# Optimization experiments

Measured on AMD Instinct MI355X. Metric: run time of the kernel, lower is better.

Reference implementation:

```python
import jax, jax.numpy as jnp
import numpy as np
from jax import lax

E = 10        # embed_dim
SEQ = 4000    # input_frame (sample_length=40)
G = 800       # group
F = 5         # frames_in_group
B = 16
VOCAB = 8192


def _conv2d(x, w, b):
    # x: [B, C, H, W], w: [O, I, 3, 3], padding=1 -> SAME
    y = lax.conv_general_dilated(x, w, (1, 1), 'SAME',
                                 dimension_numbers=('NCHW', 'OIHW', 'NCHW'))
    return y + b[None, :, None, None]


def _conv1d_k1(x, w, b):
    # Conv1d(seq, seq, kernel=1): x [B, S, L], w [S_out, S_in]
    return jnp.einsum('oi,bil->bol', w, x) + b[None, :, None]


def _linear(x, w, b):
    # torch Linear: w [out, in]
    return x @ w.T + b


def setup_inputs() -> dict:
    key = jax.random.key(0)
    ks = jax.random.split(key, 24)
    s = 0.02
    inp = {
        'X': jax.random.randint(ks[0], (B, SEQ, 15), 0, VOCAB),
        'emb_table': jax.random.normal(ks[1], (VOCAB, E), jnp.float32),
        'w_dwc_lsp': jax.random.normal(ks[2], (G, G, 3, 3), jnp.float32) * s,
        'b_dwc_lsp': jnp.zeros((G,), jnp.float32),
        'w_dwc_other': jax.random.normal(ks[3], (G, G, 3, 3), jnp.float32) * s,
        'b_dwc_other': jnp.zeros((G,), jnp.float32),
        'w_local': jax.random.normal(ks[4], (SEQ, SEQ), jnp.float32) * s,
        'b_local': jnp.zeros((SEQ,), jnp.float32),
        'w_global': jax.random.normal(ks[5], (SEQ, SEQ), jnp.float32) * s,
        'b_global': jnp.zeros((SEQ,), jnp.float32),
        'w_gq': jax.random.normal(ks[6], (4 * E, 4 * E), jnp.float32) * s,
        'b_gq': jnp.zeros((4 * E,), jnp.float32),
        'w_cq': jax.random.normal(ks[7], (4 * E, 4 * E), jnp.float32) * s,
        'b_cq': jnp.zeros((4 * E,), jnp.float32),
        'w_pq': jax.random.normal(ks[8], (4 * E, 3 * E), jnp.float32) * s,
        'b_pq': jnp.zeros((4 * E,), jnp.float32),
        'w_lk': jax.random.normal(ks[9], (4 * E, 4 * E), jnp.float32) * s,
        'b_lk': jnp.zeros((4 * E,), jnp.float32),
        'w_lv': jax.random.normal(ks[10], (4 * E, 4 * E), jnp.float32) * s,
        'b_lv': jnp.zeros((4 * E,), jnp.float32),
        'w_cls': jax.random.normal(ks[11], (1, SEQ * 4 * E * 3), jnp.float32) * 0.001,
        'b_cls': jnp.zeros((1,), jnp.float32),
        'bn_w': jnp.ones((1,), jnp.float32),
        'bn_b': jnp.zeros((1,), jnp.float32),
    }
    return inp


def reference(X, emb_table, w_dwc_lsp, b_dwc_lsp, w_dwc_other, b_dwc_other,
              w_local, b_local, w_global, b_global,
              w_gq, b_gq, w_cq, b_cq, w_pq, b_pq,
              w_lk, b_lk, w_lv, b_lv, w_cls, b_cls, bn_w, bn_b):
    batch, seq, cw = X.shape
    gamma = jnp.float32(0.8)
    pk = jnp.array([0, 0, 0, 0, 1, 3, 1, 2, 3, 2, 3, 1, 2, 3, 3], jnp.float32)
    D = jnp.repeat(gamma ** pk, E)  # [150]

    Xe = emb_table[X].reshape(batch, seq, cw * E) * D  # [B, S, 150]
    ch = Xe.reshape(batch, seq, cw, E)                  # 15 chunks of E

    lsp = ch[:, :, jnp.array([0, 1, 2, 3])].reshape(batch, seq, 4 * E)
    pitch = ch[:, :, jnp.array([4, 5, 10])].reshape(batch, seq, 3 * E)
    code = ch[:, :, jnp.array([6, 7, 11, 12])].reshape(batch, seq, 4 * E)
    gain = ch[:, :, jnp.array([8, 13, 9, 14])].reshape(batch, seq, 4 * E)

    conv_lsp = _conv2d(lsp.reshape(batch, G, F, 4 * E), w_dwc_lsp, b_dwc_lsp).reshape(batch, seq, 4 * E)
    conv_pitch = _conv2d(pitch.reshape(batch, G, F, 3 * E), w_dwc_other, b_dwc_other).reshape(batch, seq, 3 * E)
    conv_code = _conv2d(code.reshape(batch, G, F, 4 * E), w_dwc_other, b_dwc_other).reshape(batch, seq, 4 * E)
    conv_gain = _conv2d(gain.reshape(batch, G, F, 4 * E), w_dwc_other, b_dwc_other).reshape(batch, seq, 4 * E)

    conv_lsp = _conv1d_k1(conv_lsp, w_local, b_local)
    conv_pitch = _conv1d_k1(conv_pitch, w_local, b_local)
    conv_code = _conv1d_k1(conv_code, w_local, b_local)
    conv_gain = _conv1d_k1(conv_gain, w_local, b_local)

    gain_q = _linear(conv_gain, w_gq, b_gq)    # [B, S, 40]
    pitch_q = _linear(conv_pitch, w_pq, b_pq)  # [B, S, 40]
    code_q = _linear(conv_code, w_cq, b_cq)    # [B, S, 40]
    lsp_k = _linear(conv_lsp, w_lk, b_lk)
    lsp_v = _linear(conv_lsp, w_lv, b_lv)

    # Q @ K^T @ V with no softmax: associate as Q @ (K^T V), O(S*d^2)
    kv = jnp.einsum('bsd,bse->bde', lsp_k, lsp_v)  # [B, 40, 40]
    out_gain = jnp.einsum('bsd,bde->bse', gain_q, kv) + lsp
    out_pitch = jnp.einsum('bsd,bde->bse', pitch_q, kv) + lsp
    out_code = jnp.einsum('bsd,bde->bse', code_q, kv) + lsp

    atten_out = jnp.concatenate([out_gain, out_pitch, out_code], -1)  # [B, S, 120]
    gf = _conv1d_k1(atten_out, w_global, b_global).reshape(batch, -1)  # [B, 480000]

    y = gf @ w_cls.T + b_cls  # [B, 1]
    # BatchNorm1d(1) in eval mode: running_mean=0, running_var=1
    eps = jnp.float32(1e-5)
    y = y * (bn_w / jnp.sqrt(1.0 + eps)) + bn_b
    return jax.nn.sigmoid(y)
```

## Files before the change

### kernel.cpp

```cpp
#include <hip/hip_runtime.h>
#include <hip/hip_bf16.h>

typedef _Float16 f16;
typedef __attribute__((ext_vector_type(8))) _Float16 half8;
typedef __attribute__((ext_vector_type(4))) _Float16 half4;
typedef __attribute__((ext_vector_type(4))) float f32x4;

static const int BN = 16, SEQN = 4000;

__device__ __forceinline__ void gload_lds(f16* lds, const f16* g) {
  __builtin_amdgcn_global_load_lds((const __attribute__((address_space(1))) unsigned int*)g,
                                   (__attribute__((address_space(3))) unsigned int*)lds, 16, 0, 0);
}

__device__ __forceinline__ int xcd_swz(int orig, int nwg) {
  int q = nwg >> 3, r = nwg & 7, x = orig & 7, o = orig >> 3;
  return (x < r ? x * (q + 1) : r * (q + 1) + (x - r) * q) + o;
}

__device__ __forceinline__ void body_wconv(char* SM, int o,
    const float* __restrict__ w_dwc_l, f16* __restrict__ wp_lsp) {
  float* sh = (float*)SM;
  int t = threadIdx.x;
  for (int p4 = t; p4 < 1800; p4 += 256)
    *(f32x4*)&sh[p4 * 4] = *(const f32x4*)&w_dwc_l[(long)o * 7200 + p4 * 4];
  __syncthreads();
  for (int c = t; c < 912; c += 256) {
    int p = c * 8;
    int seg = p / 2432, r = p - seg * 2432;
    half8 h = {};
    if (r < 2400) {
      int de = r / 800, gib = r - de * 800;
#pragma unroll
      for (int j = 0; j < 8; j++) h[j] = (f16)sh[(gib + j) * 9 + seg * 3 + de];
    }
    *(half8*)&wp_lsp[(long)o * 7296 + p] = h;
  }
}

__device__ __forceinline__ void body_wlocal(char* SM, int s,
    const float* __restrict__ w_local, f16* __restrict__ wlp) {
  float* sh = (float*)SM;
  int t = threadIdx.x;
  for (int p = t; p < 4000; p += 256) {
    int g = p / 5, f = p - g * 5;
    sh[f * 808 + g] = w_local[(long)s * 4000 + p];
  }
  __syncthreads();
  for (int c = t; c < 512; c += 256) {
    int p = c * 8;
    half8 h = {};
    if (p < 4000) {
      int f = p / 800, g = p - f * 800;
      const float* src = &sh[f * 808 + g];
#pragma unroll
      for (int j = 0; j < 8; j++) h[j] = (f16)src[j];
    }
    *(half8*)&wlp[(long)s * 4096 + p] = h;
  }
}

__device__ __forceinline__ void body_wcT(char* SM, int id,
    const float* __restrict__ w_cls, f16* __restrict__ wcT) {
  float (*tile)[33] = (float(*)[33])SM;
  int t = threadIdx.x;
  int c0 = (id % 4) * 32, r0 = (id / 4) * 32;
  int tx = t & 31, ty = t >> 5;
  for (int i = ty; i < 32; i += 8) {
    int r = r0 + i, c = c0 + tx;
    tile[i][tx] = (r < 4000 && c < 120) ? w_cls[(long)r * 120 + c] : 0.f;
  }
  __syncthreads();
  for (int i = ty; i < 32; i += 8) {
    int c = c0 + i, r = r0 + tx;
    if (c < 128 && r < 4000) wcT[(long)c * 4000 + r] = (f16)(tile[tx][i] * 1024.f);
  }
}

__device__ __forceinline__ void body_woT(char* SM, int id,
    const float* __restrict__ in, f16* __restrict__ out) {
  float (*sh)[292] = (float(*)[292])SM;
  int bg = id % 25, bgi = id / 25;
  int g0 = bg * 32, gi0 = bgi * 32;
  int t = threadIdx.x;
  for (int p = t; p < 2304; p += 256) {
    int gl = p / 72, q4 = p % 72;
    *(f32x4*)&sh[gl][q4 * 4] = *(const f32x4*)&in[(long)(g0 + gl) * 7200 + gi0 * 9 + q4 * 4];
  }
  __syncthreads();
  for (int c = t; c < 1152; c += 256) {
    int gl8 = c & 3, q = c >> 2;
    int gil = q & 31, z = q >> 5;
    half8 h;
#pragma unroll
    for (int j = 0; j < 8; j++) h[j] = (f16)sh[gl8 * 8 + j][gil * 9 + z];
    *(half8*)&out[(long)z * 640000 + (gi0 + gil) * 800 + g0 + gl8 * 8] = h;
  }
}

__device__ __forceinline__ void body_gather(char* SM, int bid,
    const int* __restrict__ X, const float* __restrict__ emb,
    f16* __restrict__ P_lsp, f16* __restrict__ P_pit,
    f16* __restrict__ P_cod, f16* __restrict__ P_gai,
    float* __restrict__ lsp32) {
  int* sx_ = (int*)SM;
  float* slsp = (float*)(SM + 9600);
  const float scale[15] = {1.f,1.f,1.f,1.f,0.8f,0.512f,0.8f,0.64f,0.512f,0.64f,0.512f,0.8f,0.64f,0.512f,0.512f};
  const int br[15] = {0,0,0,0,1,1,2,2,3,3,1,2,2,3,3};
  const int po[15] = {0,1,2,3,0,1,0,1,0,2,2,2,3,1,3};
  int t = threadIdx.x;
  int b = bid / 25, gc = bid % 25;
  int g0 = gc * 32, s0 = g0 * 5;
  const int* xbase = X + ((long)b * SEQN + s0) * 15;
  for (int p = t; p < 600; p += 256)
    *(f32x4*)&sx_[p * 4] = *(const f32x4*)&xbase[p * 4];
  __syncthreads();
  for (int it = t; it < 2400; it += 256) {
    int gl = it & 31, q = it >> 5, f = q % 5, c = q / 5;
    int idx = sx_[(gl * 5 + f) * 15 + c];
    const float* er = emb + (long)idx * 10;
    int ty = br[c], p = po[c];
    f16* P = (ty == 0) ? P_lsp : (ty == 1) ? P_pit : (ty == 2) ? P_cod : P_gai;
    int Wp = (ty == 1) ? 32 : 42;
    f16* base = P + ((long)((f + 1) * 16 + b) * Wp + (1 + p * 10)) * 800 + g0 + gl;
    float sc = scale[c];
#pragma unroll
    for (int j = 0; j < 10; j++) {
      float v = er[j] * sc;
      base[(long)j * 800] = (f16)v;
      if (ty == 0) slsp[(gl * 5 + f) * 40 + p * 10 + j] = v;
    }
  }
  __syncthreads();
  float* ldst = lsp32 + ((long)b * SEQN + s0) * 40;
  for (int p4 = t; p4 < 1600; p4 += 256)
    *(f32x4*)&ldst[p4 * 4] = *(const f32x4*)&slsp[p4 * 4];
}

__device__ __forceinline__ void body_c1(char* SM, int blk,
    const float* __restrict__ wcls, const float* __restrict__ bg,
    float* __restrict__ c1p) {
  float* red = (float*)SM;
  int t = threadIdx.x;
  float s = 0.f;
  for (long i = (long)blk * 256 + t; i < 480000; i += (long)120 * 256)
    s += wcls[i] * bg[i / 120];
  red[t] = s; __syncthreads();
  for (int o = 128; o > 0; o >>= 1) { if (t < o) red[t] += red[t + o]; __syncthreads(); }
  if (t == 0) c1p[blk] = red[0];
}

__device__ __forceinline__ void body_conv(char* SM, int id,
    const f16* __restrict__ P, const f16* __restrict__ wp, f16* __restrict__ Cp) {
  f16* Asb = (f16*)SM;
  f16* Bsb = Asb + 8192;
  int lin = xcd_swz(id % 175, 175);
  int z = id / 175;
  int df = z >> 1, hf = z & 1;
  int nx = lin % 7, my = lin / 7;
  int m0 = my * 128, n0 = nx * 128;
  Cp += (long)z * 2560000;
  int t = threadIdx.x;
  int gslot = (t & 3) ^ ((t >> 3) & 3);
  const f16 *ap[2], *bp[2];
#pragma unroll
  for (int q = 0; q < 2; q++) {
    int row = q * 64 + (t >> 2);
    int m = m0 + row;
    int f = m / 640, rem = m % 640, b = rem / 40, e = rem % 40;
    ap[q] = P + ((long)((f + df) * 16 + b) * 42 + e) * 800 + hf * 1216 + gslot * 8;
    bp[q] = wp + (long)(n0 + row) * 7296 + df * 2432 + hf * 1216 + gslot * 8;
  }
  int lane = t & 63, wv = t >> 6, l15 = lane & 15, kg = lane >> 4;
  int wm = (wv >> 1) * 64, wn = (wv & 1) * 64;
  int so = (kg ^ ((l15 >> 1) & 3)) << 3;
  f32x4 acc[4][4] = {};
  gload_lds(&Asb[t * 8], ap[0]); gload_lds(&Asb[2048 + t * 8], ap[1]);
  gload_lds(&Bsb[t * 8], bp[0]); gload_lds(&Bsb[2048 + t * 8], bp[1]);
  __syncthreads();
  int cur = 0;
  for (int kt = 0; kt < 38; kt++) {
    if (kt + 1 < 38) {
      int o = (kt + 1) * 32, nb = cur ^ 1;
      gload_lds(&Asb[nb * 4096 + t * 8], ap[0] + o); gload_lds(&Asb[nb * 4096 + 2048 + t * 8], ap[1] + o);
      gload_lds(&Bsb[nb * 4096 + t * 8], bp[0] + o); gload_lds(&Bsb[nb * 4096 + 2048 + t * 8], bp[1] + o);
    }
    half8 av[4], bv[4];
#pragma unroll
    for (int i = 0; i < 4; i++) av[i] = *(const half8*)&Asb[cur * 4096 + (wm + i * 16 + l15) * 32 + so];
#pragma unroll
    for (int j = 0; j < 4; j++) bv[j] = *(const half8*)&Bsb[cur * 4096 + (wn + j * 16 + l15) * 32 + so];
#pragma unroll
    for (int i = 0; i < 4; i++)
#pragma unroll
      for (int j = 0; j < 4; j++)
        acc[i][j] = __builtin_amdgcn_mfma_f32_16x16x32_f16(av[i], bv[j], acc[i][j], 0, 0, 0);
    __syncthreads();
    cur ^= 1;
  }
#pragma unroll
  for (int i = 0; i < 4; i++) {
    int mb = m0 + wm + i * 16 + kg * 4;
#pragma unroll
    for (int j = 0; j < 4; j++) {
      int n = n0 + wn + j * 16 + l15;
      if (n >= 800) continue;
      f32x4 d = acc[i][j];
#pragma unroll
      for (int r = 0; r < 4; r++)
        Cp[(long)(mb + r) * 800 + n] = (f16)d[r];
    }
  }
}

template <int OUTF16>
__device__ __forceinline__ void body_gemm128(char* SM, int x, int ky, int z,
    const f16* __restrict__ A, int lda, const f16* __restrict__ Bm, int ldb,
    float* __restrict__ C, f16* __restrict__ C16, int ldc,
    int gx, int nwg, int nkt, int KTtot, long cslice, long az, long bz, long cz,
    int Mreal, int Nreal, int Aclamp) {
  f16* Asb = (f16*)SM;
  f16* Bsb = Asb + 8192;
  A += (long)z * az;
  Bm += (long)z * bz;
  if (OUTF16) C16 += (long)z * cz + (long)ky * cslice;
  else C += (long)z * cz + (long)ky * cslice;
  int lin = xcd_swz(x, nwg);
  int nx = lin % gx, my = lin / gx;
  int m0 = my * 128, n0 = nx * 128;
  int kt0 = ky * nkt;
  int ktn = nkt; if (kt0 + ktn > KTtot) ktn = KTtot - kt0;
  int t = threadIdx.x;
  int gslot = (t & 3) ^ ((t >> 3) & 3);
  const f16 *ap[2], *bp[2];
#pragma unroll
  for (int q = 0; q < 2; q++) {
    int row = q * 64 + (t >> 2);
    int ra = m0 + row; if (ra >= Aclamp) ra = Aclamp - 1;
    ap[q] = A + (long)ra * lda + (long)kt0 * 32 + gslot * 8;
    bp[q] = Bm + (long)(n0 + row) * ldb + (long)kt0 * 32 + gslot * 8;
  }
  int lane = t & 63, wv = t >> 6, l15 = lane & 15, kg = lane >> 4;
  int wm = (wv >> 1) * 64, wn = (wv & 1) * 64;
  int so = (kg ^ ((l15 >> 1) & 3)) << 3;
  f32x4 acc[4][4] = {};
  gload_lds(&Asb[t * 8], ap[0]); gload_lds(&Asb[2048 + t * 8], ap[1]);
  gload_lds(&Bsb[t * 8], bp[0]); gload_lds(&Bsb[2048 + t * 8], bp[1]);
  __syncthreads();
  int cur = 0;
  for (int kt = 0; kt < ktn; kt++) {
    if (kt + 1 < ktn) {
      int o = (kt + 1) * 32, nb = cur ^ 1;
      gload_lds(&Asb[nb * 4096 + t * 8], ap[0] + o); gload_lds(&Asb[nb * 4096 + 2048 + t * 8], ap[1] + o);
      gload_lds(&Bsb[nb * 4096 + t * 8], bp[0] + o); gload_lds(&Bsb[nb * 4096 + 2048 + t * 8], bp[1] + o);
    }
    half8 av[4], bv[4];
#pragma unroll
    for (int i = 0; i < 4; i++) av[i] = *(const half8*)&Asb[cur * 4096 + (wm + i * 16 + l15) * 32 + so];
#pragma unroll
    for (int j = 0; j < 4; j++) bv[j] = *(const half8*)&Bsb[cur * 4096 + (wn + j * 16 + l15) * 32 + so];
#pragma unroll
    for (int i = 0; i < 4; i++)
#pragma unroll
      for (int j = 0; j < 4; j++)
        acc[i][j] = __builtin_amdgcn_mfma_f32_16x16x32_f16(av[i], bv[j], acc[i][j], 0, 0, 0);
    __syncthreads();
    cur ^= 1;
  }
#pragma unroll
  for (int i = 0; i < 4; i++) {
    int mb = m0 + wm + i * 16 + kg * 4;
#pragma unroll
    for (int j = 0; j < 4; j++) {
      int n = n0 + wn + j * 16 + l15;
      if (n >= Nreal) continue;
      f32x4 d = acc[i][j];
#pragma unroll
      for (int r = 0; r < 4; r++) {
        int m = mb + r;
        if (m >= Mreal) continue;
        if (OUTF16) C16[(long)m * ldc + n] = (f16)d[r];
        else C[(long)m * ldc + n] = d[r];
      }
    }
  }
}

__device__ __forceinline__ void body_tn(char* SM, int id,
    const f16* __restrict__ A, int lda, const float* __restrict__ B, int ldb,
    float* __restrict__ C, int ldc, int nkt, int KTtot, long cslice,
    int Mreal, int Nreal) {
  f16* As = (f16*)SM;
  f16* Bs = As + 4096;
  int n0 = (id & 31) * 128;
  int ky = id >> 5;
  int kt0 = ky * nkt;
  int ktn = nkt; if (kt0 + ktn > KTtot) ktn = KTtot - kt0;
  C += (long)ky * cslice;
  int t = threadIdx.x;
  int gslot = (t & 3) ^ ((t >> 3) & 3);
  const f16 *ap0, *ap1;
  {
    int r0 = t >> 2, r1 = 64 + (t >> 2);
    if (r0 >= Mreal) r0 = Mreal - 1;
    if (r1 >= Mreal) r1 = Mreal - 1;
    ap0 = A + (long)r0 * lda + (long)kt0 * 32 + gslot * 8;
    ap1 = A + (long)r1 * lda + (long)kt0 * 32 + gslot * 8;
  }
  int lane = t & 63, wv = t >> 6;
  int wm = (wv >> 1) * 64, wn = (wv & 1) * 64;
  int l15 = lane & 15, kg = lane >> 4;
  int so = (kg ^ ((l15 >> 1) & 3)) << 3;
  f32x4 acc[4][4] = {};
  for (int kt = 0; kt < ktn; kt++) {
    float rb[4][4];
    int nli[4], kqi[4];
#pragma unroll
    for (int i = 0; i < 4; i++) {
      int idd = i * 256 + t;
      nli[i] = idd & 127; kqi[i] = idd >> 7;
      int gn = n0 + nli[i]; if (gn >= Nreal) gn = Nreal - 1;
      long kb = ((long)(kt0 + kt) * 32 + kqi[i] * 4);
#pragma unroll
      for (int j = 0; j < 4; j++) rb[i][j] = B[(kb + j) * ldb + gn];
    }
    __syncthreads();
    gload_lds(&As[t * 8], ap0 + kt * 32);
    gload_lds(&As[2048 + t * 8], ap1 + kt * 32);
#pragma unroll
    for (int i = 0; i < 4; i++) {
      half4 h = {(f16)rb[i][0], (f16)rb[i][1], (f16)rb[i][2], (f16)rb[i][3]};
      *(half4*)&Bs[nli[i] * 36 + kqi[i] * 4] = h;
    }
    __syncthreads();
    half8 av[4], bv[4];
#pragma unroll
    for (int i = 0; i < 4; i++) {
      av[i] = *(const half8*)(&As[(wm + i * 16 + l15) * 32 + so]);
      bv[i] = *(const half8*)(&Bs[(wn + i * 16 + l15) * 36 + kg * 8]);
    }
#pragma unroll
    for (int i = 0; i < 4; i++)
#pragma unroll
      for (int j = 0; j < 4; j++)
        acc[i][j] = __builtin_amdgcn_mfma_f32_16x16x32_f16(av[i], bv[j], acc[i][j], 0, 0, 0);
  }
#pragma unroll
  for (int i = 0; i < 4; i++) {
    int mb = wm + i * 16 + kg * 4;
#pragma unroll
    for (int j = 0; j < 4; j++) {
      int n = n0 + wn + j * 16 + l15;
      if (n >= Nreal) continue;
      f32x4 d = acc[i][j];
#pragma unroll
      for (int r = 0; r < 4; r++) {
        int m = mb + r;
        if (m >= Mreal) continue;
        C[(long)m * ldc + n] = d[r];
      }
    }
  }
}

__device__ __forceinline__ void body_co_red(long gid,
    const f16* __restrict__ Cp, const float* __restrict__ bias, f16* __restrict__ co) {
  if (gid >= 640000) return;
  int m = gid / 200, n4 = (gid % 200) * 4;
  long o = (long)m * 800 + n4;
  f32x4 s = *(const f32x4*)&bias[n4];
#pragma unroll
  for (int z = 0; z < 6; z++) {
    half4 h = *(const half4*)&Cp[(long)z * 2560000 + o];
    s += (f32x4){(float)h[0], (float)h[1], (float)h[2], (float)h[3]};
  }
  int f = m / 640, r2 = m % 640;
  half4 hh = {(f16)s[0], (f16)s[1], (f16)s[2], (f16)s[3]};
  *(half4*)&co[(long)r2 * 4000 + f * 800 + n4] = hh;
}

__device__ __forceinline__ void body_vred(int idb, int MODE,
    const float* __restrict__ vp, float* __restrict__ vout, f16* __restrict__ tout) {
  int x = idb & 15, ec = idb >> 4;
  int s = x * 256 + threadIdx.x;
  if (s >= 4000) return;
  int g = s / 5, f = s % 5;
  float sums[40];
#pragma unroll
  for (int eo = 0; eo < 40; eo++) {
    int e = ec * 40 + eo;
    float sum = 0.f;
#pragma unroll
    for (int z = 0; z < 10; z++) sum += vp[(long)z * 480000 + (long)e * 4000 + s];
    sums[eo] = sum;
    if (MODE == 0) tout[(long)e * 4000 + s] = (f16)sum;
    else tout[(long)(f * 120 + e) * 832 + g] = (f16)sum;
  }
#pragma unroll
  for (int q = 0; q < 10; q++)
    *(f32x4*)&vout[(long)s * 120 + ec * 40 + q * 4] = *(f32x4*)&sums[q * 4];
}

__device__ __forceinline__ void body_cl_red(long gid,
    const f16* __restrict__ Clp, const float* __restrict__ bl, float* __restrict__ cl) {
  if (gid >= 640000) return;
  int m = gid / 160, n4 = (gid % 160) * 4;
  long o = (long)m * 640 + n4;
  float b = bl[m];
  f32x4 s = {b, b, b, b};
#pragma unroll
  for (int z = 0; z < 4; z++) {
    half4 h = *(const half4*)&Clp[(long)z * 2560000 + o];
    s += (f32x4){(float)h[0], (float)h[1], (float)h[2], (float)h[3]};
  }
  *(f32x4*)&cl[o] = s;
}

__device__ __forceinline__ void body_resid(char* SM, int chunk, int b,
    const float* __restrict__ lsp32, const float* __restrict__ vmat,
    float* __restrict__ rpart) {
  float* red = (float*)SM;
  int t = threadIdx.x;
  int s0 = chunk * 160;
  float y = 0.f;
  for (int idx = t; idx < 1600; idx += 256) {
    int sr = idx / 10, d4 = idx % 10;
    const float* lp = lsp32 + ((long)b * SEQN + s0 + sr) * 40 + d4 * 4;
    const float* vp = vmat + (long)(s0 + sr) * 120 + d4 * 4;
    f32x4 l = *(const f32x4*)lp;
    f32x4 vs = *(const f32x4*)vp + *(const f32x4*)(vp + 40) + *(const f32x4*)(vp + 80);
    y += l[0] * vs[0] + l[1] * vs[1] + l[2] * vs[2] + l[3] * vs[3];
  }
  red[t] = y; __syncthreads();
  for (int o = 128; o > 0; o >>= 1) { if (t < o) red[t] += red[t + o]; __syncthreads(); }
  if (t == 0) rpart[b * 25 + chunk] = red[0];
}

__device__ __forceinline__ void body_kv(char* SM, int chunk, int b,
    const float* __restrict__ cl, const float* __restrict__ wlk, const float* __restrict__ blk,
    const float* __restrict__ wlv, const float* __restrict__ blv, float* __restrict__ kvp) {
  float* s_wk = (float*)SM;
  float* s_wv = s_wk + 1600;
  float* s_cl = s_wv + 1600;
  float* s_k  = s_cl + 320;
  float* s_v  = s_k + 320;
  int t = threadIdx.x;
  for (int p = t; p < 1600; p += 256) { s_wk[p] = wlk[p]; s_wv[p] = wlv[p]; }
  float acc[7] = {0.f, 0.f, 0.f, 0.f, 0.f, 0.f, 0.f};
  for (int c8 = 0; c8 < 20; c8++) {
    int sb = chunk * 160 + c8 * 8;
    __syncthreads();
    for (int p = t; p < 320; p += 256) {
      int sl = p / 40, e = p % 40;
      s_cl[sl * 40 + e] = cl[(long)(sb + sl) * 640 + b * 40 + e];
    }
    __syncthreads();
    for (int p = t; p < 640; p += 256) {
      int half = p / 320, q = p % 320, sl = q / 40, d = q % 40;
      const float* w = half ? s_wv : s_wk;
      float r = half ? blv[d] : blk[d];
      for (int e = 0; e < 40; e++) r += w[d * 40 + e] * s_cl[sl * 40 + e];
      if (half) s_v[sl * 40 + d] = r; else s_k[sl * 40 + d] = r;
    }
    __syncthreads();
    int ai = 0;
    for (int p = t; p < 1600; p += 256, ai++) {
      int d = p / 40, e = p % 40;
      float a = acc[ai];
      for (int sl = 0; sl < 8; sl++) a += s_k[sl * 40 + d] * s_v[sl * 40 + e];
      acc[ai] = a;
    }
  }
  int ai = 0;
  for (int p = t; p < 1600; p += 256, ai++)
    kvp[((long)(b * 25 + chunk)) * 1600 + p] = acc[ai];
}

__device__ __forceinline__ void body_consts(char* SM, int e,
    const float* __restrict__ Vt, const float* __restrict__ vmat,
    const float* __restrict__ bconv, const float* __restrict__ blocal,
    float* __restrict__ cbblv, float* __restrict__ svv) {
  float* r1 = (float*)SM;
  float* r2 = r1 + 256;
  int t = threadIdx.x;
  float a = 0.f, b = 0.f;
  for (int s = t; s < 4000; s += 256) {
    a += bconv[s / 5] * Vt[(long)s * 120 + e] + blocal[s] * vmat[(long)s * 120 + e];
    b += vmat[(long)s * 120 + e];
  }
  r1[t] = a; r2[t] = b; __syncthreads();
  for (int o = 128; o > 0; o >>= 1) {
    if (t < o) { r1[t] += r1[t + o]; r2[t] += r2[t + o]; }
    __syncthreads();
  }
  if (t == 0) { cbblv[e] = r1[0]; svv[e] = r2[0]; }
}

__device__ __forceinline__ void body_fold(long c8,
    const float* __restrict__ A9, f16* __restrict__ Bp) {
  long p = c8 * 8;
  if (p >= 7 * 120 * 2496) return;
  int fp = p / 299520;
  int r = p % 299520;
  int eg = r / 2496, k2 = r % 2496;
  int zk = k2 / 832, kk = k2 % 832;
  half8 h = {};
  if (kk < 800) {
#pragma unroll
    for (int j = 0; j < 8; j++) {
      float s = 0.f;
#pragma unroll
      for (int dh = 0; dh < 3; dh++) {
        int f = fp - dh;
        if (f >= 0 && f < 5)
          s += A9[((long)(dh * 3 + zk) * 640 + f * 120 + eg) * 800 + kk + j];
      }
      h[j] = (f16)s;
    }
  }
  *(half8*)&Bp[p] = h;
}

__device__ __forceinline__ void body_kvred(long gid,
    const float* __restrict__ kvp, float* __restrict__ kv) {
  if (gid >= 16 * 1600) return;
  int b = gid / 1600, p = gid % 1600;
  float s = 0.f;
  for (int c = 0; c < 25; c++) s += kvp[((long)(b * 25 + c)) * 1600 + p];
  kv[gid] = s;
}

__device__ __forceinline__ void body_U(char* SM, int id,
    const f16* __restrict__ Pg, const f16* __restrict__ Pp, const f16* __restrict__ Pc,
    const f16* __restrict__ Bp, float* __restrict__ Upart) {
  f16* Asb = (f16*)SM;
  f16* Bsb = Asb + 8192;
  int m0 = (id % 28) * 64;
  int y = id / 28, fp = y / 3, zk = y % 3;
  const f16* P; int seg0, jw, Wp, e0;
  if (m0 < 640)       { seg0 = 0;    jw = 40; Wp = 42; e0 = 0;  P = Pg; }
  else if (m0 < 1152) { seg0 = 640;  jw = 30; Wp = 32; e0 = 40; P = Pp; }
  else                { seg0 = 1152; jw = 40; Wp = 42; e0 = 80; P = Pc; }
  P += (long)fp * 16 * Wp * 800;
  int t = threadIdx.x;
  int gslot = (t & 7) ^ ((t >> 3) & 7);
  const f16 *ap[2], *bp[2];
#pragma unroll
  for (int q = 0; q < 2; q++) {
    int row = q * 32 + (t >> 3);
    int l = m0 + row - seg0; if (l >= 16 * jw) l = 0;
    ap[q] = P + ((long)(l / jw) * Wp + (l % jw)) * 800 + (long)zk * 800 + gslot * 8;
    int brow = row; if (e0 + brow > 119) brow = 119 - e0;
    bp[q] = Bp + ((long)fp * 120 + e0 + brow) * 2496 + zk * 832 + gslot * 8;
  }
  int lane = t & 63, wv = t >> 6, l15 = lane & 15, kg = lane >> 4;
  int sx = l15 & 7;
  f32x4 acc[3] = {};
  gload_lds(&Asb[t * 8], ap[0]); gload_lds(&Asb[2048 + t * 8], ap[1]);
  gload_lds(&Bsb[t * 8], bp[0]); gload_lds(&Bsb[2048 + t * 8], bp[1]);
  __syncthreads();
  int cur = 0;
  for (int kt = 0; kt < 13; kt++) {
    if (kt + 1 < 13) {
      int o = (kt + 1) * 64, nb = cur ^ 1;
      gload_lds(&Asb[nb * 4096 + t * 8], ap[0] + o); gload_lds(&Asb[nb * 4096 + 2048 + t * 8], ap[1] + o);
      gload_lds(&Bsb[nb * 4096 + t * 8], bp[0] + o); gload_lds(&Bsb[nb * 4096 + 2048 + t * 8], bp[1] + o);
    }
#pragma unroll
    for (int ks = 0; ks < 2; ks++) {
      int so = ((ks * 4 + kg) ^ sx) << 3;
      half8 av = *(const half8*)&Asb[cur * 4096 + (wv * 16 + l15) * 64 + so];
#pragma unroll
      for (int j = 0; j < 3; j++) {
        half8 bv = *(const half8*)&Bsb[cur * 4096 + (j * 16 + l15) * 64 + so];
        acc[j] = __builtin_amdgcn_mfma_f32_16x16x32_f16(av, bv, acc[j], 0, 0, 0);
      }
    }
    __syncthreads();
    cur ^= 1;
  }
#pragma unroll
  for (int j = 0; j < 3; j++) {
    int n = j * 16 + l15;
    if (n >= 40) continue;
    f32x4 d = acc[j];
#pragma unroll
    for (int r = 0; r < 4; r++) {
      int m = m0 + wv * 16 + kg * 4 + r;
      if (m - seg0 >= 16 * jw) continue;
      Upart[((long)y * 1792 + m) * 40 + n] = d[r];
    }
  }
}

__device__ __forceinline__ void body_ured(long gid,
    const float* __restrict__ Upart, const float* __restrict__ cbblv,
    float* __restrict__ Ufin) {
  if (gid >= 1792 * 40) return;
  int m = gid / 40, e = gid % 40;
  int e0 = m < 640 ? 0 : (m < 1152 ? 40 : 80);
  float s = cbblv[e0 + e];
  for (int y = 0; y < 21; y++) s += Upart[(long)y * 71680 + gid];
  Ufin[gid] = s;
}

__global__ __launch_bounds__(256) void k_phase0(
    const float* w_dwc_l, f16* wp_lsp, const float* w_cls, f16* wcT,
    const int* X, const float* emb, f16* P_lsp, f16* P_pit, f16* P_cod, f16* P_gai,
    float* lsp32, const float* b_global, float* c1p) {
  __shared__ __align__(16) char SM[35200];
  int bid = blockIdx.x;
  if (bid < 800) body_wconv(SM, bid, w_dwc_l, wp_lsp);
  else if (bid < 1300) body_wcT(SM, bid - 800, w_cls, wcT);
  else if (bid < 1700) body_gather(SM, bid - 1300, X, emb, P_lsp, P_pit, P_cod, P_gai, lsp32);
  else body_c1(SM, bid - 1700, w_cls, b_global, c1p);
}

__global__ __launch_bounds__(256) void k_phase1(
    const f16* P_lsp, const f16* wp_lsp, f16* Cp,
    const f16* wcT, const float* w_global, float* vpart,
    const float* w_local, f16* wlp) {
  __shared__ __align__(16) char SM[32768];
  int bid = blockIdx.x;
  if (bid < 1050) body_conv(SM, bid, P_lsp, wp_lsp, Cp);
  else if (bid < 1370) body_tn(SM, bid - 1050, wcT, 4000, w_global, 4000, vpart, 4000, 13, 125, 480000L, 120, 4000);
  else body_wlocal(SM, bid - 1370, w_local, wlp);
}

__global__ __launch_bounds__(256) void k_phase2(
    const f16* Cp, const float* b_dwc_l, f16* co,
    const float* vpart, float* vmat, f16* vT,
    const float* w_dwc_o, f16* woT) {
  __shared__ __align__(16) char SM[37376];
  int bid = blockIdx.x;
  if (bid < 2500) body_co_red((long)bid * 256 + threadIdx.x, Cp, b_dwc_l, co);
  else if (bid < 2548) body_vred(bid - 2500, 0, vpart, vmat, vT);
  else body_woT(SM, bid - 2548, w_dwc_o, woT);
}

__global__ __launch_bounds__(256) void k_phase3(
    const f16* wlp, const f16* co, f16* Clp,
    const f16* vT, const float* w_local, float* vpart,
    const float* lsp32, const float* vmat, float* rpart) {
  __shared__ __align__(16) char SM[32768];
  int bid = blockIdx.x;
  if (bid < 640) body_gemm128<1>(SM, bid % 160, bid / 160, 0, wlp, 4096, co, 4000, nullptr, Clp, 640,
                                 5, 160, 32, 128, 2560000L, 0, 0, 0, 4000, 640, 4000);
  else if (bid < 960) body_tn(SM, bid - 640, vT, 4000, w_local, 4000, vpart, 4000, 13, 125, 480000L, 120, 4000);
  else { int id = bid - 960; body_resid(SM, id % 25, id / 25, lsp32, vmat, rpart); }
}

__global__ __launch_bounds__(256) void k_phase4(
    const f16* Clp, const float* b_local, float* cl,
    const float* vpart, float* Vt, f16* vtT) {
  int bid = blockIdx.x;
  if (bid < 2500) body_cl_red((long)bid * 256 + threadIdx.x, Clp, b_local, cl);
  else body_vred(bid - 2500, 1, vpart, Vt, vtT);
}

__global__ __launch_bounds__(256) void k_phase5(
    const float* cl, const float* w_lk, const float* b_lk,
    const float* w_lv, const float* b_lv, float* kvp,
    const f16* vtT, const f16* woT, float* A9,
    const float* Vt, const float* vmat, const float* b_dwc_o, const float* b_local,
    float* cbblv, float* svv) {
  __shared__ __align__(16) char SM[32768];
  int bid = blockIdx.x;
  if (bid < 400) body_kv(SM, bid % 25, bid / 25, cl, w_lk, b_lk, w_lv, b_lv, kvp);
  else if (bid < 715) { int id = bid - 400; body_gemm128<0>(SM, id % 35, 0, id / 35, vtT, 832, woT, 800, A9, nullptr, 800,
                                                             7, 35, 26, 26, 0L, 0, 640000, 512000, 600, 800, 600); }
  else body_consts(SM, bid - 715, Vt, vmat, b_dwc_o, b_local, cbblv, svv);
}

__global__ __launch_bounds__(256) void k_phase6(
    const float* A9, f16* Bp, const float* kvp, float* kvb) {
  int bid = blockIdx.x;
  if (bid < 1024) body_fold((long)bid * 256 + threadIdx.x, A9, Bp);
  else body_kvred((long)(bid - 1024) * 256 + threadIdx.x, kvp, kvb);
}

__global__ __launch_bounds__(256) void k_phase7(
    const f16* P_gai, const f16* P_pit, const f16* P_cod,
    const f16* Bp, float* Upart) {
  __shared__ __align__(16) char SM[32768];
  body_U(SM, blockIdx.x, P_gai, P_pit, P_cod, Bp, Upart);
}

__global__ __launch_bounds__(256) void k_phase8(
    const float* Upart, const float* cbblv, float* Ufin) {
  body_ured((long)blockIdx.x * 256 + threadIdx.x, Upart, cbblv, Ufin);
}

__global__ __launch_bounds__(256) void k_final(
    const float* __restrict__ Ufin, const float* __restrict__ kvb,
    const float* __restrict__ rpart,
    const float* __restrict__ wgq, const float* __restrict__ wpq, const float* __restrict__ wcq,
    const float* __restrict__ bgq, const float* __restrict__ bpq, const float* __restrict__ bcq,
    const float* __restrict__ svv, const float* __restrict__ c1p,
    const float* __restrict__ bcls, const float* __restrict__ bnw,
    const float* __restrict__ bnb, float* __restrict__ out) {
  __shared__ float s_kv[1600], s_U[4800], s_w[4400], s_bq[120], s_sv[120], s_red[256];
  int b = blockIdx.x, t = threadIdx.x;
  for (int p = t; p < 1600; p += 256) {
    s_kv[p] = kvb[b * 1600 + p];
    s_w[p] = wgq[p];
    s_w[2800 + p] = wcq[p];
  }
  for (int p = t; p < 1200; p += 256) s_w[1600 + p] = wpq[p];
  for (int p = t; p < 4800; p += 256) {
    int tt = p / 1600, r = p % 1600, j = r / 40, e = r % 40;
    float uv = 0.f;
    if (tt == 0) uv = Ufin[(b * 40 + j) * 40 + e];
    else if (tt == 1) { if (j < 30) uv = Ufin[(640 + b * 30 + j) * 40 + e]; }
    else uv = Ufin[(1152 + b * 40 + j) * 40 + e];
    s_U[p] = uv;
  }
  if (t < 40) { s_bq[t] = bgq[t]; s_bq[40 + t] = bpq[t]; s_bq[80 + t] = bcq[t]; }
  for (int p = t; p < 120; p += 256) s_sv[p] = svv[p];
  __syncthreads();
  float y = 0.f;
  for (int p = t; p < 4800; p += 256) {
    int tt = p / 1600, q = p % 1600, d = q / 40, e = q % 40;
    float T = 0.f;
    if (tt == 0) {
      for (int j = 0; j < 40; j++) T += s_w[d * 40 + j] * s_U[j * 40 + e];
    } else if (tt == 1) {
      for (int j = 0; j < 30; j++) T += s_w[1600 + d * 30 + j] * s_U[1600 + j * 40 + e];
    } else {
      for (int j = 0; j < 40; j++) T += s_w[2800 + d * 40 + j] * s_U[3200 + j * 40 + e];
    }
    y += s_kv[d * 40 + e] * (T + s_bq[tt * 40 + d] * s_sv[tt * 40 + e]);
  }
  for (int p = t; p < 25; p += 256) y += rpart[b * 25 + p];
  s_red[t] = y; __syncthreads();
  for (int o = 128; o > 0; o >>= 1) { if (t < o) s_red[t] += s_red[t + o]; __syncthreads(); }
  if (t == 0) {
    float c1 = bcls[0];
    for (int i = 0; i < 120; i++) c1 += c1p[i];
    float yy = s_red[0] * (1.f / 1024.f) + c1;
    yy = yy * (bnw[0] * rsqrtf(1.f + 1e-5f)) + bnb[0];
    out[b] = 1.f / (1.f + expf(-yy));
  }
}

extern "C" void kernel_launch(void* const* d_in, const int* in_sizes, int n_in,
                              void* d_out, int out_size, void* d_ws, size_t ws_size,
                              hipStream_t stream) {
  const int*   X        = (const int*)d_in[0];
  const float* emb      = (const float*)d_in[1];
  const float* w_dwc_l  = (const float*)d_in[2];
  const float* b_dwc_l  = (const float*)d_in[3];
  const float* w_dwc_o  = (const float*)d_in[4];
  const float* b_dwc_o  = (const float*)d_in[5];
  const float* w_local  = (const float*)d_in[6];
  const float* b_local  = (const float*)d_in[7];
  const float* w_global = (const float*)d_in[8];
  const float* b_global = (const float*)d_in[9];
  const float* w_gq = (const float*)d_in[10];
  const float* b_gq = (const float*)d_in[11];
  const float* w_cq = (const float*)d_in[12];
  const float* b_cq = (const float*)d_in[13];
  const float* w_pq = (const float*)d_in[14];
  const float* b_pq = (const float*)d_in[15];
  const float* w_lk = (const float*)d_in[16];
  const float* b_lk = (const float*)d_in[17];
  const float* w_lv = (const float*)d_in[18];
  const float* b_lv = (const float*)d_in[19];
  const float* w_cls = (const float*)d_in[20];
  const float* b_cls = (const float*)d_in[21];
  const float* bn_w = (const float*)d_in[22];
  const float* bn_b = (const float*)d_in[23];
  float* out = (float*)d_out;

  char* ws = (char*)d_ws;
  size_t off = 0;
  auto alloc = [&](size_t bytes) -> void* {
    off = (off + 255) & ~(size_t)255;
    void* p = ws + off; off += bytes; return p;
  };

  const size_t sz_p40 = (size_t)7 * 16 * 42 * 800 * 2;
  const size_t sz_p30 = (size_t)7 * 16 * 32 * 800 * 2;
  f16* P_lsp = (f16*)alloc(sz_p40 + 256);
  f16* P_pit = (f16*)alloc(sz_p30 + 256);
  f16* P_cod = (f16*)alloc(sz_p40 + 256);
  f16* P_gai = (f16*)alloc(sz_p40 + 256);
  float* lsp32 = (float*)alloc((size_t)16 * 4000 * 40 * 4);
  f16* wp_lsp = (f16*)alloc((size_t)896 * 7296 * 2);
  f16* wlp    = (f16*)alloc((size_t)4000 * 4096 * 2 + 256);
  f16* wcT    = (f16*)alloc((size_t)128 * 4000 * 2);
  f16* vT     = (f16*)alloc((size_t)128 * 4000 * 2);
  f16* co     = (f16*)alloc((size_t)640 * 4000 * 2 + 256);
  float* cl   = (float*)alloc((size_t)4000 * 640 * 4);
  float* vmat  = (float*)alloc((size_t)480000 * 4);
  float* Vt    = (float*)alloc((size_t)480000 * 4);
  f16* vtT   = (f16*)alloc((size_t)640 * 832 * 2 + 256);
  f16* Bp    = (f16*)alloc((size_t)7 * 120 * 2496 * 2);
  float* Upart = (float*)alloc((size_t)21 * 1792 * 40 * 4);
  float* Ufin  = (float*)alloc((size_t)1792 * 40 * 4);
  float* cbblv = (float*)alloc(120 * 4);
  float* svv   = (float*)alloc(120 * 4);
  float* kvp  = (float*)alloc((size_t)400 * 1600 * 4);
  float* kvb  = (float*)alloc((size_t)16 * 1600 * 4);
  float* c1p  = (float*)alloc(120 * 4);
  float* rpart = (float*)alloc(400 * 4);
  f16* woT = (f16*)alloc(((size_t)9 * 640000 + 76800) * 2);
  float* vpart = (float*)alloc((size_t)10 * 480000 * 4);
  char* arena = (char*)alloc((size_t)32 * 1024 * 1024);
  f16* Cp   = (f16*)arena;
  f16* Clp  = (f16*)arena;
  float* A9 = (float*)arena;
  (void)ws_size; (void)in_sizes; (void)n_in; (void)out_size;

  hipMemsetAsync(P_lsp, 0, sz_p40, stream);
  hipMemsetAsync(P_pit, 0, sz_p30, stream);
  hipMemsetAsync(P_cod, 0, sz_p40, stream);
  hipMemsetAsync(P_gai, 0, sz_p40, stream);
  hipMemsetAsync(vtT, 0, (size_t)640 * 832 * 2, stream);

  k_phase0<<<1820, 256, 0, stream>>>(w_dwc_l, wp_lsp, w_cls, wcT,
                                     X, emb, P_lsp, P_pit, P_cod, P_gai,
                                     lsp32, b_global, c1p);
  k_phase1<<<5370, 256, 0, stream>>>(P_lsp, wp_lsp, Cp, wcT, w_global, vpart,
                                     w_local, wlp);
  k_phase2<<<3173, 256, 0, stream>>>(Cp, b_dwc_l, co, vpart, vmat, vT, w_dwc_o, woT);
  k_phase3<<<1360, 256, 0, stream>>>(wlp, co, Clp, vT, w_local, vpart, lsp32, vmat, rpart);
  k_phase4<<<2548, 256, 0, stream>>>(Clp, b_local, cl, vpart, Vt, vtT);
  k_phase5<<<835, 256, 0, stream>>>(cl, w_lk, b_lk, w_lv, b_lv, kvp,
                                    vtT, woT, A9, Vt, vmat, b_dwc_o, b_local, cbblv, svv);
  k_phase6<<<1124, 256, 0, stream>>>(A9, Bp, kvp, kvb);
  k_phase7<<<588, 256, 0, stream>>>(P_gai, P_pit, P_cod, Bp, Upart);
  k_phase8<<<280, 256, 0, stream>>>(Upart, cbblv, Ufin);
  k_final<<<16, 256, 0, stream>>>(Ufin, kvb, rpart,
                                  w_gq, w_pq, w_cq, b_gq, b_pq, b_cq,
                                  svv, c1p, b_cls, bn_w, bn_b, out);
}
```

Measured before the change: 445.5 us.

## Hoist weight conversions into phase0 and reuse fp16 w_local in TN GEMM

Moves the w_local fp16 pack (wlp) and the w_dwc_other transpose (woT) into the first phase kernel, so later phases only run compute and reductions. The phase-3 TN GEMM now reads the already-converted fp16 wlp instead of fp32 w_local, halving that operand's bytes. The vred column index changes to match the wlp layout. Phase0 becomes a much larger launch, which may lengthen the critical path before phase1 starts.

```diff
diff --git a/kernel.cpp b/kernel.cpp
--- a/kernel.cpp
+++ b/kernel.cpp
@@ -287,7 +287,8 @@
 }
 
 __device__ __forceinline__ void body_tn(char* SM, int id,
-    const f16* __restrict__ A, int lda, const float* __restrict__ B, int ldb,
+    const f16* __restrict__ A, int lda, const float* __restrict__ B,
+    const f16* __restrict__ B16, int ldb,
     float* __restrict__ C, int ldc, int nkt, int KTtot, long cslice,
     int Mreal, int Nreal) {
   f16* As = (f16*)SM;
@@ -313,7 +314,7 @@
   int so = (kg ^ ((l15 >> 1) & 3)) << 3;
   f32x4 acc[4][4] = {};
   for (int kt = 0; kt < ktn; kt++) {
-    float rb[4][4];
+    f16 rb[4][4];
     int nli[4], kqi[4];
 #pragma unroll
     for (int i = 0; i < 4; i++) {
@@ -322,14 +323,15 @@
       int gn = n0 + nli[i]; if (gn >= Nreal) gn = Nreal - 1;
       long kb = ((long)(kt0 + kt) * 32 + kqi[i] * 4);
 #pragma unroll
-      for (int j = 0; j < 4; j++) rb[i][j] = B[(kb + j) * ldb + gn];
+      for (int j = 0; j < 4; j++)
+        rb[i][j] = B16 ? B16[(kb + j) * ldb + gn] : (f16)B[(kb + j) * ldb + gn];
     }
     __syncthreads();
     gload_lds(&As[t * 8], ap0 + kt * 32);
     gload_lds(&As[2048 + t * 8], ap1 + kt * 32);
 #pragma unroll
     for (int i = 0; i < 4; i++) {
-      half4 h = {(f16)rb[i][0], (f16)rb[i][1], (f16)rb[i][2], (f16)rb[i][3]};
+      half4 h = {rb[i][0], rb[i][1], rb[i][2], rb[i][3]};
       *(half4*)&Bs[nli[i] * 36 + kqi[i] * 4] = h;
     }
     __syncthreads();
@@ -385,13 +387,14 @@
   int s = x * 256 + threadIdx.x;
   if (s >= 4000) return;
   int g = s / 5, f = s % 5;
+  int scol = (MODE == 0) ? s : (f * 800 + g);
   float sums[40];
 #pragma unroll
   for (int eo = 0; eo < 40; eo++) {
     int e = ec * 40 + eo;
     float sum = 0.f;
 #pragma unroll
-    for (int z = 0; z < 10; z++) sum += vp[(long)z * 480000 + (long)e * 4000 + s];
+    for (int z = 0; z < 10; z++) sum += vp[(long)z * 480000 + (long)e * 4000 + scol];
     sums[eo] = sum;
     if (MODE == 0) tout[(long)e * 4000 + s] = (f16)sum;
     else tout[(long)(f * 120 + e) * 832 + g] = (f16)sum;
@@ -605,48 +608,47 @@
 }
 
 __global__ __launch_bounds__(256) void k_phase0(
-    const float* w_dwc_l, f16* wp_lsp, const float* w_cls, f16* wcT,
+    const float* w_local, f16* wlp, const float* w_dwc_l, f16* wp_lsp,
+    const float* w_cls, f16* wcT,
     const int* X, const float* emb, f16* P_lsp, f16* P_pit, f16* P_cod, f16* P_gai,
-    float* lsp32, const float* b_global, float* c1p) {
-  __shared__ __align__(16) char SM[35200];
+    float* lsp32, const float* b_global, float* c1p,
+    const float* w_dwc_o, f16* woT) {
+  __shared__ __align__(16) char SM[37376];
   int bid = blockIdx.x;
-  if (bid < 800) body_wconv(SM, bid, w_dwc_l, wp_lsp);
-  else if (bid < 1300) body_wcT(SM, bid - 800, w_cls, wcT);
-  else if (bid < 1700) body_gather(SM, bid - 1300, X, emb, P_lsp, P_pit, P_cod, P_gai, lsp32);
-  else body_c1(SM, bid - 1700, w_cls, b_global, c1p);
+  if (bid < 4000) body_wlocal(SM, bid, w_local, wlp);
+  else if (bid < 4800) body_wconv(SM, bid - 4000, w_dwc_l, wp_lsp);
+  else if (bid < 5300) body_wcT(SM, bid - 4800, w_cls, wcT);
+  else if (bid < 5700) body_gather(SM, bid - 5300, X, emb, P_lsp, P_pit, P_cod, P_gai, lsp32);
+  else if (bid < 5820) body_c1(SM, bid - 5700, w_cls, b_global, c1p);
+  else body_woT(SM, bid - 5820, w_dwc_o, woT);
 }
 
 __global__ __launch_bounds__(256) void k_phase1(
     const f16* P_lsp, const f16* wp_lsp, f16* Cp,
-    const f16* wcT, const float* w_global, float* vpart,
-    const float* w_local, f16* wlp) {
+    const f16* wcT, const float* w_global, float* vpart) {
   __shared__ __align__(16) char SM[32768];
   int bid = blockIdx.x;
   if (bid < 1050) body_conv(SM, bid, P_lsp, wp_lsp, Cp);
-  else if (bid < 1370) body_tn(SM, bid - 1050, wcT, 4000, w_global, 4000, vpart, 4000, 13, 125, 480000L, 120, 4000);
-  else body_wlocal(SM, bid - 1370, w_local, wlp);
+  else body_tn(SM, bid - 1050, wcT, 4000, w_global, nullptr, 4000, vpart, 4000, 13, 125, 480000L, 120, 4000);
 }
 
 __global__ __launch_bounds__(256) void k_phase2(
     const f16* Cp, const float* b_dwc_l, f16* co,
-    const float* vpart, float* vmat, f16* vT,
-    const float* w_dwc_o, f16* woT) {
-  __shared__ __align__(16) char SM[37376];
+    const float* vpart, float* vmat, f16* vT) {
   int bid = blockIdx.x;
   if (bid < 2500) body_co_red((long)bid * 256 + threadIdx.x, Cp, b_dwc_l, co);
-  else if (bid < 2548) body_vred(bid - 2500, 0, vpart, vmat, vT);
-  else body_woT(SM, bid - 2548, w_dwc_o, woT);
+  else body_vred(bid - 2500, 0, vpart, vmat, vT);
 }
 
 __global__ __launch_bounds__(256) void k_phase3(
     const f16* wlp, const f16* co, f16* Clp,
-    const f16* vT, const float* w_local, float* vpart,
+    const f16* vT, float* vpart,
     const float* lsp32, const float* vmat, float* rpart) {
   __shared__ __align__(16) char SM[32768];
   int bid = blockIdx.x;
   if (bid < 640) body_gemm128<1>(SM, bid % 160, bid / 160, 0, wlp, 4096, co, 4000, nullptr, Clp, 640,
                                  5, 160, 32, 128, 2560000L, 0, 0, 0, 4000, 640, 4000);
-  else if (bid < 960) body_tn(SM, bid - 640, vT, 4000, w_local, 4000, vpart, 4000, 13, 125, 480000L, 120, 4000);
+  else if (bid < 960) body_tn(SM, bid - 640, vT, 4000, nullptr, wlp, 4096, vpart, 4000, 13, 125, 480000L, 120, 4000);
   else { int id = bid - 960; body_resid(SM, id % 25, id / 25, lsp32, vmat, rpart); }
 }
 
@@ -818,13 +820,12 @@
   hipMemsetAsync(P_gai, 0, sz_p40, stream);
   hipMemsetAsync(vtT, 0, (size_t)640 * 832 * 2, stream);
 
-  k_phase0<<<1820, 256, 0, stream>>>(w_dwc_l, wp_lsp, w_cls, wcT,
+  k_phase0<<<6445, 256, 0, stream>>>(w_local, wlp, w_dwc_l, wp_lsp, w_cls, wcT,
                                      X, emb, P_lsp, P_pit, P_cod, P_gai,
-                                     lsp32, b_global, c1p);
-  k_phase1<<<5370, 256, 0, stream>>>(P_lsp, wp_lsp, Cp, wcT, w_global, vpart,
-                                     w_local, wlp);
-  k_phase2<<<3173, 256, 0, stream>>>(Cp, b_dwc_l, co, vpart, vmat, vT, w_dwc_o, woT);
-  k_phase3<<<1360, 256, 0, stream>>>(wlp, co, Clp, vT, w_local, vpart, lsp32, vmat, rpart);
+                                     lsp32, b_global, c1p, w_dwc_o, woT);
+  k_phase1<<<1370, 256, 0, stream>>>(P_lsp, wp_lsp, Cp, wcT, w_global, vpart);
+  k_phase2<<<2548, 256, 0, stream>>>(Cp, b_dwc_l, co, vpart, vmat, vT);
+  k_phase3<<<1360, 256, 0, stream>>>(wlp, co, Clp, vT, vpart, lsp32, vmat, rpart);
   k_phase4<<<2548, 256, 0, stream>>>(Clp, b_local, cl, vpart, Vt, vtT);
   k_phase5<<<835, 256, 0, stream>>>(cl, w_lk, b_lk, w_lv, b_lv, kvp,
                                     vtT, woT, A9, Vt, vmat, b_dwc_o, b_local, cbblv, svv);
```

New measurement: 475.1 us. 1.07x slower.
